# Kernel tuning notes

Hardware: AMD Instinct MI355X
Metric: run time of the kernel (lower is better)

Reference implementation:

```python
import jax, jax.numpy as jnp
import numpy as np
from jax import lax

H = 250  # hidden size of all LSTM layers


def _lstm_layer(x, Wih, Whh, bih, bhh):
    """Single-layer LSTM over time-major x [T, in], batch=1 folded away.
    PyTorch gate order: i, f, g, o. Returns hidden states [T, H]."""
    b = bih + bhh
    # Precompute input projections for all timesteps (parallel GEMM)
    xW = x @ Wih.T + b  # [T, 4H]

    def step(carry, xw_t):
        h, c = carry
        gates = xw_t + h @ Whh.T  # [4H]
        i, f, g, o = jnp.split(gates, 4)
        i = jax.nn.sigmoid(i)
        f = jax.nn.sigmoid(f)
        g = jnp.tanh(g)
        o = jax.nn.sigmoid(o)
        c = f * c + i * g
        h = o * jnp.tanh(c)
        return (h, c), h

    h0 = jnp.zeros((Whh.shape[1],), x.dtype)
    (_, _), hs = lax.scan(step, (h0, h0), xW)
    return hs  # [T, H]


def setup_inputs() -> dict:
    key = jax.random.key(0)
    ks = jax.random.split(key, 16)
    T, D = 8192, 1
    s = 1.0 / np.sqrt(H)  # PyTorch default uniform(-1/sqrt(H), 1/sqrt(H))
    u = lambda k, shape: jax.random.uniform(k, shape, jnp.float32, -s, s)
    inp = {
        "input_seq": jax.random.normal(ks[0], (T, D), jnp.float32),
        # lstm (2 layers), layer 0: input_size=1
        "Wih0": u(ks[1], (4 * H, D)), "Whh0": u(ks[2], (4 * H, H)),
        "bih0": u(ks[3], (4 * H,)), "bhh0": u(ks[4], (4 * H,)),
        # lstm layer 1: input=H
        "Wih1": u(ks[5], (4 * H, H)), "Whh1": u(ks[6], (4 * H, H)),
        "bih1": u(ks[7], (4 * H,)), "bhh1": u(ks[8], (4 * H,)),
        # lstm_1 (1 layer): input=H
        "Wih2": u(ks[9], (4 * H, H)), "Whh2": u(ks[10], (4 * H, H)),
        "bih2": u(ks[11], (4 * H,)), "bhh2": u(ks[12], (4 * H,)),
        # final linear H -> 1
        "Wl": u(ks[13], (1, H)), "bl": u(ks[14], (1,)),
    }
    return inp


def reference(input_seq, Wih0, Whh0, bih0, bhh0, Wih1, Whh1, bih1, bhh1,
              Wih2, Whh2, bih2, bhh2, Wl, bl):
    T = input_seq.shape[0]
    x = input_seq.reshape(T, -1)            # [T, 1] (batch=1 squeezed)
    h0 = _lstm_layer(x, Wih0, Whh0, bih0, bhh0)   # stacked LSTM layer 0
    h1 = _lstm_layer(h0, Wih1, Whh1, bih1, bhh1)  # layer 1 (dropout=0.2 inactive at eval)
    h2 = _lstm_layer(h1, Wih2, Whh2, bih2, bhh2)  # second LSTM module
    preds = h2 @ Wl.T + bl                  # [T, 1]
    return preds[-1]                        # [1]
```

## Files before the change

kernel.cpp:

```cpp
#include <hip/hip_runtime.h>
#include <cstdint>

#define HDIM 250
#define GDIM 1000
#define CH   64
#define PP   4
#define HRING 4
#define XRING 4
#define RPAD 1024
#define NTH  512

#define W_LDS_QPT 18
#define LDSW_BYTES (W_LDS_QPT * NTH * 16)
#define HSEG 144
#define HBUF (4 * HSEG)
#define HB_BASE LDSW_BYTES
#define RED_BASE (HB_BASE + 2 * HBUF)
#define SMEM_BYTES (RED_BASE + 1024)

typedef _Float16 f16x2 __attribute__((ext_vector_type(2)));

__device__ __forceinline__ float fdot2u(uint32_t w, uint32_t h, float acc) {
#if defined(__has_builtin) && __has_builtin(__builtin_amdgcn_fdot2)
  return __builtin_amdgcn_fdot2(__builtin_bit_cast(f16x2, w),
                                __builtin_bit_cast(f16x2, h), acc, false);
#else
  f16x2 wv = __builtin_bit_cast(f16x2, w), hv = __builtin_bit_cast(f16x2, h);
  return acc + (float)wv[0] * (float)hv[0] + (float)wv[1] * (float)hv[1];
#endif
}

__device__ __forceinline__ uint32_t pkh2(float a, float b) {
  f16x2 p; p[0] = (_Float16)a; p[1] = (_Float16)b;
  return __builtin_bit_cast(uint32_t, p);
}

__device__ __forceinline__ uint4 pack8q(const float* rp, int c0) {
  float c[8];
#pragma unroll
  for (int u = 0; u < 8; ++u) {
    int col = c0 + u;
    c[u] = (rp && col < HDIM) ? rp[col] : 0.f;
  }
  uint4 r;
  r.x = pkh2(c[0], c[1]); r.y = pkh2(c[2], c[3]);
  r.z = pkh2(c[4], c[5]); r.w = pkh2(c[6], c[7]);
  return r;
}

__device__ __forceinline__ float sigm(float x) {
  return 1.f / (1.f + exp2f(-1.44269504088896341f * x));
}
__device__ __forceinline__ float tanh_(float x) {
  float e = exp2f(2.88539008177792681f * x);
  return 1.f - 2.f / (e + 1.f);
}

template <int CTRL>
__device__ __forceinline__ float dppq(float v) {
  return __builtin_bit_cast(
      float, __builtin_amdgcn_update_dpp(0, __builtin_bit_cast(int, v), CTRL,
                                         0xF, 0xF, true));
}

__device__ __forceinline__ constexpr int kv_count(int r) { return r < 6 ? 6 : 5; }
__device__ __forceinline__ constexpr int wv_idx(int r, int k) {
  return r < 6 ? r * 6 + k : 36 + (r - 6) * 5 + k;
}
__device__ __forceinline__ constexpr int wl_idx(int r, int k) {
  return r < 6 ? r * 2 + (k - 6) : 12 + (r - 6) * 3 + (k - 5);
}

__device__ __forceinline__ void step_barrier() {
  asm volatile("s_waitcnt lgkmcnt(0)\n\ts_barrier" ::: "memory");
}

#define F_HCNT(F, li)     (F)[(li)]
#define F_XWCON(F, li)    (F)[2 + (li)]
#define F_HDONE(F, li, p) (F)[4 + (li) * PP + (p)]
#define F_XWRDY(F, li, c) (F)[16 + (li) * 128 + (c)]

__device__ __forceinline__ int aload(int* p) {
  return __hip_atomic_load(p, __ATOMIC_RELAXED, __HIP_MEMORY_SCOPE_AGENT);
}
__device__ __forceinline__ void arel(int* p, int v) {
  __hip_atomic_store(p, v, __ATOMIC_RELEASE, __HIP_MEMORY_SCOPE_AGENT);
}
__device__ __forceinline__ void acq_fence() {
  __builtin_amdgcn_fence(__ATOMIC_ACQUIRE, "agent");
}
__device__ __forceinline__ void spin_ge(int* p, int tgt) {
  unsigned n = 0;
  while (aload(p) < tgt) {
    __builtin_amdgcn_s_sleep(2);
    if (++n > 200000000u) return;
  }
}

__global__ void lstm_init(const float* __restrict__ Wih1, const float* __restrict__ bih1,
                          const float* __restrict__ bhh1, const float* __restrict__ Wih2,
                          const float* __restrict__ bih2, const float* __restrict__ bhh2,
                          float* __restrict__ WT, float* __restrict__ BV) {
  int idx = blockIdx.x * blockDim.x + threadIdx.x;
  int stride = gridDim.x * blockDim.x;
  for (int i = idx; i < 2 * HDIM * RPAD; i += stride) {
    int li = i / (HDIM * RPAD);
    int rem = i - li * HDIM * RPAD;
    int j = rem / RPAD, r = rem - j * RPAD;
    const float* W = li ? Wih2 : Wih1;
    WT[i] = (r < GDIM) ? W[r * HDIM + j] : 0.f;
  }
  for (int i = idx; i < 2 * RPAD; i += stride) {
    int li = i >> 10, r = i & 1023;
    const float* bi = li ? bih2 : bih1;
    const float* bh = li ? bhh2 : bhh1;
    BV[i] = (r < GDIM) ? bi[r] + bh[r] : 0.f;
  }
}

__global__ __launch_bounds__(512, 2) void lstm_main(
    const float* __restrict__ x, const float* __restrict__ Wih0,
    const float* __restrict__ bih0, const float* __restrict__ bhh0,
    const float* __restrict__ Whh0, const float* __restrict__ Whh1,
    const float* __restrict__ Whh2, const float* __restrict__ Wl,
    const float* __restrict__ bl, int* __restrict__ F,
    const float* __restrict__ WT, const float* __restrict__ BV,
    float* __restrict__ hRing, float* __restrict__ xwRing,
    float* __restrict__ out, int T) {
  extern __shared__ char smem[];
  const int tid = threadIdx.x;
  const int bid = blockIdx.x;
  const int NC = T / CH;

  if (bid < 3) {
    const int L = bid;
    const int grp = tid >> 2, sl = tid & 3;
    const bool lead = (sl < 2);
    const int uu = 2 * grp + sl;

    const float* Whh = (L == 0) ? Whh0 : (L == 1) ? Whh1 : Whh2;
    uint4 wv[46];
    {
#pragma unroll
      for (int r = 0; r < 8; ++r) {
        const int w = r >> 2, gate = r & 3;
        const int u = 2 * grp + w;
        const float* rp = (u < HDIM) ? (Whh + (size_t)(gate * HDIM + u) * HDIM) : nullptr;
#pragma unroll
        for (int k = 0; k < 8; ++k) {
          uint4 q = pack8q(rp, sl * 64 + k * 8);
          if (k < kv_count(r)) wv[wv_idx(r, k)] = q;
          else *(uint4*)(smem + (size_t)(wl_idx(r, k) * NTH + tid) * 16) = q;
        }
      }
    }
    for (int i = tid; i < (2 * HBUF) / 4; i += NTH)
      *(uint32_t*)(smem + HB_BASE + 4 * i) = 0u;
    __syncthreads();

    const float* xwBase = xwRing + (size_t)(L > 0 ? L - 1 : 0) * XRING * CH * RPAD;
    float* hBase = hRing + (size_t)L * HRING * CH * HDIM;
    float c_st = 0.f, h_last = 0.f;

    for (int tt = 0; tt < T; ++tt) {
      const int tc = tt & (CH - 1);
      const int c = tt >> 6;
      if (tc == 0) {
        if (tid == 0) {
          if (L > 0) spin_ge(&F_XWRDY(F, L - 1, c), 1);
          if (L < 2 && c >= HRING) {
            int cc = c - HRING;
            spin_ge(&F_HDONE(F, L, cc % PP), cc + 1);
          }
          acq_fence();
        }
        __syncthreads();
      }

      float xw0 = 0.f, xw1 = 0.f, xw2 = 0.f, xw3 = 0.f;
      if (lead && uu < HDIM) {
        if (L == 0) {
          float xt = x[tt];
          xw0 = fmaf(xt, Wih0[uu], bih0[uu] + bhh0[uu]);
          xw1 = fmaf(xt, Wih0[250 + uu], bih0[250 + uu] + bhh0[250 + uu]);
          xw2 = fmaf(xt, Wih0[500 + uu], bih0[500 + uu] + bhh0[500 + uu]);
          xw3 = fmaf(xt, Wih0[750 + uu], bih0[750 + uu] + bhh0[750 + uu]);
        } else {
          const float* xp = xwBase + (size_t)(c & (XRING - 1)) * CH * RPAD +
                            (size_t)tc * RPAD;
          xw0 = xp[uu]; xw1 = xp[250 + uu]; xw2 = xp[500 + uu]; xw3 = xp[750 + uu];
        }
      }

      step_barrier();

      const char* hb = smem + HB_BASE + (tt & 1) * HBUF + sl * HSEG;
      float acc[8] = {0.f, 0.f, 0.f, 0.f, 0.f, 0.f, 0.f, 0.f};
#pragma unroll
      for (int k = 0; k < 8; ++k) {
        const uint4 hq = *(const uint4*)(hb + k * 16);
#pragma unroll
        for (int r = 0; r < 8; ++r) {
          uint4 wq = (k < kv_count(r))
                         ? wv[wv_idx(r, k)]
                         : *(const uint4*)(smem + (size_t)(wl_idx(r, k) * NTH + tid) * 16);
          acc[r] = fdot2u(wq.x, hq.x, acc[r]);
          acc[r] = fdot2u(wq.y, hq.y, acc[r]);
          acc[r] = fdot2u(wq.z, hq.z, acc[r]);
          acc[r] = fdot2u(wq.w, hq.w, acc[r]);
        }
      }
#pragma unroll
      for (int r = 0; r < 8; ++r) {
        acc[r] += dppq<0xB1>(acc[r]);
        acc[r] += dppq<0x4E>(acc[r]);
      }

      if (lead) {
        const int of = sl * 4;
        float gi = acc[of + 0] + xw0, gf = acc[of + 1] + xw1;
        float gG = acc[of + 2] + xw2, go = acc[of + 3] + xw3;
        float ii = sigm(gi), ff = sigm(gf), tg = tanh_(gG), oo = sigm(go);
        c_st = ff * c_st + ii * tg;
        float hn = oo * tanh_(c_st);
        h_last = hn;
        float hOther = dppq<0xB1>(hn);
        if (sl == 0) {
          char* hw = smem + HB_BASE + ((tt + 1) & 1) * HBUF + (uu >> 6) * HSEG +
                     (uu & 63) * 2;
          *(uint32_t*)hw = pkh2(hn, hOther);
          if (L < 2 && uu < HDIM) {
            float2 hp; hp.x = hn; hp.y = hOther;
            *(float2*)(hBase + (size_t)(c & (HRING - 1)) * CH * HDIM +
                       (size_t)tc * HDIM + uu) = hp;
          }
        }
      }

      if (tc == CH - 1) {
        __syncthreads();
        if (tid == 0) {
          if (L < 2) arel(&F_HCNT(F, L), c + 1);
          if (L > 0) arel(&F_XWCON(F, L - 1), c + 1);
        }
      }
    }

    if (L == 2) {
      float* red = (float*)(smem + RED_BASE);
      if (lead && uu < HDIM) red[uu] = h_last;
      __syncthreads();
      if (tid == 0) {
        float s = bl[0];
        for (int j = 0; j < HDIM; ++j) s += red[j] * Wl[j];
        out[0] = s;
      }
    }
  } else {
    const int li = (bid - 3) / PP;
    const int p = (bid - 3) % PP;
    float* ldsH = (float*)smem;
    const int lane = tid & 63, wid = tid >> 6;
    const float* WTl = WT + (size_t)li * HDIM * RPAD;
    const float* BVl = BV + (size_t)li * RPAD;

    for (int c = p; c < NC; c += PP) {
      if (tid == 0) {
        spin_ge(&F_HCNT(F, li), c + 1);
        if (c >= XRING) spin_ge(&F_XWCON(F, li), c - XRING + 1);
        acq_fence();
      }
      __syncthreads();
      const float* hsrc = hRing + (size_t)li * HRING * CH * HDIM +
                          (size_t)(c & (HRING - 1)) * CH * HDIM;
      for (int t = wid; t < CH; t += 8)
        for (int j = lane; j < HDIM; j += 64)
          ldsH[t * 257 + j] = hsrc[t * HDIM + j];
      __syncthreads();
      if (tid == 0) arel(&F_HDONE(F, li, p), c + 1);

      float* xdst = xwRing + (size_t)li * XRING * CH * RPAD +
                    (size_t)(c & (XRING - 1)) * CH * RPAD;
      const int rb0 = wid * 128;
      for (int grpq = 0; grpq < 16; ++grpq) {
        const int rb = rb0 + grpq * 8;
        float acc[8];
#pragma unroll
        for (int u = 0; u < 8; ++u) acc[u] = 0.f;
        const float* wp = WTl + rb;
        float4 wa = *(const float4*)(wp);
        float4 wb = *(const float4*)(wp + 4);
        for (int j = 0; j < HDIM; ++j) {
          int jn = (j + 1 < HDIM) ? j + 1 : HDIM - 1;
          float4 na = *(const float4*)(wp + (size_t)jn * RPAD);
          float4 nb = *(const float4*)(wp + (size_t)jn * RPAD + 4);
          float hj = ldsH[lane * 257 + j];
          acc[0] = fmaf(wa.x, hj, acc[0]); acc[1] = fmaf(wa.y, hj, acc[1]);
          acc[2] = fmaf(wa.z, hj, acc[2]); acc[3] = fmaf(wa.w, hj, acc[3]);
          acc[4] = fmaf(wb.x, hj, acc[4]); acc[5] = fmaf(wb.y, hj, acc[5]);
          acc[6] = fmaf(wb.z, hj, acc[6]); acc[7] = fmaf(wb.w, hj, acc[7]);
          wa = na; wb = nb;
        }
#pragma unroll
        for (int u = 0; u < 8; ++u) {
          int r = rb + u;
          if (r < GDIM) xdst[(size_t)lane * RPAD + r] = acc[u] + BVl[r];
        }
      }
      __syncthreads();
      if (tid == 0) arel(&F_XWRDY(F, li, c), 1);
    }
  }
}

extern "C" void kernel_launch(void* const* d_in, const int* in_sizes, int n_in,
                              void* d_out, int out_size, void* d_ws, size_t ws_size,
                              hipStream_t stream) {
  const float* x    = (const float*)d_in[0];
  const float* Wih0 = (const float*)d_in[1];
  const float* Whh0 = (const float*)d_in[2];
  const float* bih0 = (const float*)d_in[3];
  const float* bhh0 = (const float*)d_in[4];
  const float* Wih1 = (const float*)d_in[5];
  const float* Whh1 = (const float*)d_in[6];
  const float* bih1 = (const float*)d_in[7];
  const float* bhh1 = (const float*)d_in[8];
  const float* Wih2 = (const float*)d_in[9];
  const float* Whh2 = (const float*)d_in[10];
  const float* bih2 = (const float*)d_in[11];
  const float* bhh2 = (const float*)d_in[12];
  const float* Wl   = (const float*)d_in[13];
  const float* bl   = (const float*)d_in[14];
  const int T = in_sizes[0];

  char* ws = (char*)d_ws;
  int*   F   = (int*)ws;
  float* WT  = (float*)(ws + 4096);
  float* BV  = (float*)(ws + 4096 + 2048000);
  float* hR  = (float*)(ws + 4096 + 2048000 + 8192);
  float* xwR = (float*)(ws + 4096 + 2048000 + 8192 + 512000);

  hipMemsetAsync(F, 0, 4096, stream);
  lstm_init<<<256, 256, 0, stream>>>(Wih1, bih1, bhh1, Wih2, bih2, bhh2, WT, BV);
  hipFuncSetAttribute(reinterpret_cast<const void*>(lstm_main),
                      hipFuncAttributeMaxDynamicSharedMemorySize, SMEM_BYTES);
  lstm_main<<<3 + 2 * PP, 512, SMEM_BYTES, stream>>>(
      x, Wih0, bih0, bhh0, Whh0, Whh1, Whh2, Wl, bl, F, WT, BV, hR, xwR,
      (float*)d_out, T);
}
```

Measured before the change: 21.01 ms.

## Double threads per block so each recurrent thread owns one gate row

After: 19.85 ms. -5.5%, faster.

```diff
diff --git a/kernel.cpp b/kernel.cpp
--- a/kernel.cpp
+++ b/kernel.cpp
@@ -8,10 +8,10 @@
 #define HRING 4
 #define XRING 4
 #define RPAD 1024
-#define NTH  512
-
-#define W_LDS_QPT 18
-#define LDSW_BYTES (W_LDS_QPT * NTH * 16)
+#define NTH  1024
+
+#define LQ_N 8
+#define LDSW_BYTES (LQ_N * NTH * 16)
 #define HSEG 144
 #define HBUF (4 * HSEG)
 #define HB_BASE LDSW_BYTES
@@ -48,12 +48,19 @@
   return r;
 }
 
+__device__ __forceinline__ float rcpf_(float x) {
+#if defined(__has_builtin) && __has_builtin(__builtin_amdgcn_rcpf)
+  return __builtin_amdgcn_rcpf(x);
+#else
+  return 1.f / x;
+#endif
+}
 __device__ __forceinline__ float sigm(float x) {
-  return 1.f / (1.f + exp2f(-1.44269504088896341f * x));
+  return rcpf_(1.f + exp2f(-1.44269504088896341f * x));
 }
 __device__ __forceinline__ float tanh_(float x) {
   float e = exp2f(2.88539008177792681f * x);
-  return 1.f - 2.f / (e + 1.f);
+  return 1.f - 2.f * rcpf_(e + 1.f);
 }
 
 template <int CTRL>
@@ -61,14 +68,6 @@
   return __builtin_bit_cast(
       float, __builtin_amdgcn_update_dpp(0, __builtin_bit_cast(int, v), CTRL,
                                          0xF, 0xF, true));
-}
-
-__device__ __forceinline__ constexpr int kv_count(int r) { return r < 6 ? 6 : 5; }
-__device__ __forceinline__ constexpr int wv_idx(int r, int k) {
-  return r < 6 ? r * 6 + k : 36 + (r - 6) * 5 + k;
-}
-__device__ __forceinline__ constexpr int wl_idx(int r, int k) {
-  return r < 6 ? r * 2 + (k - 6) : 12 + (r - 6) * 3 + (k - 5);
 }
 
 __device__ __forceinline__ void step_barrier() {
@@ -118,7 +117,7 @@
   }
 }
 
-__global__ __launch_bounds__(512, 2) void lstm_main(
+__global__ void __launch_bounds__(NTH) lstm_main(
     const float* __restrict__ x, const float* __restrict__ Wih0,
     const float* __restrict__ bih0, const float* __restrict__ bhh0,
     const float* __restrict__ Whh0, const float* __restrict__ Whh1,
@@ -134,26 +133,36 @@
 
   if (bid < 3) {
     const int L = bid;
-    const int grp = tid >> 2, sl = tid & 3;
-    const bool lead = (sl < 2);
-    const int uu = 2 * grp + sl;
+    const int u = tid >> 2, sl = tid & 3;
+    const bool uok = (u < HDIM);
+    const int r_abs = sl * HDIM + u;
 
     const float* Whh = (L == 0) ? Whh0 : (L == 1) ? Whh1 : Whh2;
-    uint4 wv[46];
-    {
-#pragma unroll
-      for (int r = 0; r < 8; ++r) {
-        const int w = r >> 2, gate = r & 3;
-        const int u = 2 * grp + w;
-        const float* rp = (u < HDIM) ? (Whh + (size_t)(gate * HDIM + u) * HDIM) : nullptr;
-#pragma unroll
-        for (int k = 0; k < 8; ++k) {
-          uint4 q = pack8q(rp, sl * 64 + k * 8);
-          if (k < kv_count(r)) wv[wv_idx(r, k)] = q;
-          else *(uint4*)(smem + (size_t)(wl_idx(r, k) * NTH + tid) * 16) = q;
-        }
-      }
+    char* lw = smem + tid * 16;
+#define LWADDR(lq) (lw + (size_t)(lq) * (NTH * 16))
+#define ROWP(r) (uok ? (Whh + ((size_t)(r) * HDIM + u) * HDIM) : (const float*)nullptr)
+
+    uint4 w00, w01, w02, w03, w04, w05;
+    uint4 w10, w11, w12, w13, w14, w15;
+    uint4 w20, w21, w22, w23, w24, w25;
+    uint4 w30, w31, w32, w33, w34, w35;
+#define INITROW(r)                                          \
+  w##r##0 = pack8q(ROWP(r), sl * 64 + 0);                   \
+  w##r##1 = pack8q(ROWP(r), sl * 64 + 8);                   \
+  w##r##2 = pack8q(ROWP(r), sl * 64 + 16);                  \
+  w##r##3 = pack8q(ROWP(r), sl * 64 + 24);                  \
+  w##r##4 = pack8q(ROWP(r), sl * 64 + 32);                  \
+  w##r##5 = pack8q(ROWP(r), sl * 64 + 40);                  \
+  *(uint4*)LWADDR(2 * (r)) = pack8q(ROWP(r), sl * 64 + 48); \
+  *(uint4*)LWADDR(2 * (r) + 1) = pack8q(ROWP(r), sl * 64 + 56);
+    INITROW(0) INITROW(1) INITROW(2) INITROW(3)
+
+    float w0_ = 0.f, b0_ = 0.f;
+    if (L == 0 && uok) {
+      w0_ = Wih0[r_abs];
+      b0_ = bih0[r_abs] + bhh0[r_abs];
     }
+
     for (int i = tid; i < (2 * HBUF) / 4; i += NTH)
       *(uint32_t*)(smem + HB_BASE + 4 * i) = 0u;
     __syncthreads();
@@ -177,64 +186,70 @@
         __syncthreads();
       }
 
-      float xw0 = 0.f, xw1 = 0.f, xw2 = 0.f, xw3 = 0.f;
-      if (lead && uu < HDIM) {
+      float xw = 0.f;
+      if (uok) {
         if (L == 0) {
-          float xt = x[tt];
-          xw0 = fmaf(xt, Wih0[uu], bih0[uu] + bhh0[uu]);
-          xw1 = fmaf(xt, Wih0[250 + uu], bih0[250 + uu] + bhh0[250 + uu]);
-          xw2 = fmaf(xt, Wih0[500 + uu], bih0[500 + uu] + bhh0[500 + uu]);
-          xw3 = fmaf(xt, Wih0[750 + uu], bih0[750 + uu] + bhh0[750 + uu]);
+          xw = fmaf(x[tt], w0_, b0_);
         } else {
           const float* xp = xwBase + (size_t)(c & (XRING - 1)) * CH * RPAD +
                             (size_t)tc * RPAD;
-          xw0 = xp[uu]; xw1 = xp[250 + uu]; xw2 = xp[500 + uu]; xw3 = xp[750 + uu];
-        }
-      }
-
-      step_barrier();
+          xw = xp[r_abs];
+        }
+      }
 
       const char* hb = smem + HB_BASE + (tt & 1) * HBUF + sl * HSEG;
-      float acc[8] = {0.f, 0.f, 0.f, 0.f, 0.f, 0.f, 0.f, 0.f};
-#pragma unroll
-      for (int k = 0; k < 8; ++k) {
-        const uint4 hq = *(const uint4*)(hb + k * 16);
-#pragma unroll
-        for (int r = 0; r < 8; ++r) {
-          uint4 wq = (k < kv_count(r))
-                         ? wv[wv_idx(r, k)]
-                         : *(const uint4*)(smem + (size_t)(wl_idx(r, k) * NTH + tid) * 16);
-          acc[r] = fdot2u(wq.x, hq.x, acc[r]);
-          acc[r] = fdot2u(wq.y, hq.y, acc[r]);
-          acc[r] = fdot2u(wq.z, hq.z, acc[r]);
-          acc[r] = fdot2u(wq.w, hq.w, acc[r]);
-        }
-      }
-#pragma unroll
-      for (int r = 0; r < 8; ++r) {
-        acc[r] += dppq<0xB1>(acc[r]);
-        acc[r] += dppq<0x4E>(acc[r]);
-      }
-
-      if (lead) {
-        const int of = sl * 4;
-        float gi = acc[of + 0] + xw0, gf = acc[of + 1] + xw1;
-        float gG = acc[of + 2] + xw2, go = acc[of + 3] + xw3;
-        float ii = sigm(gi), ff = sigm(gf), tg = tanh_(gG), oo = sigm(go);
-        c_st = ff * c_st + ii * tg;
-        float hn = oo * tanh_(c_st);
-        h_last = hn;
-        float hOther = dppq<0xB1>(hn);
-        if (sl == 0) {
-          char* hw = smem + HB_BASE + ((tt + 1) & 1) * HBUF + (uu >> 6) * HSEG +
-                     (uu & 63) * 2;
-          *(uint32_t*)hw = pkh2(hn, hOther);
-          if (L < 2 && uu < HDIM) {
-            float2 hp; hp.x = hn; hp.y = hOther;
-            *(float2*)(hBase + (size_t)(c & (HRING - 1)) * CH * HDIM +
-                       (size_t)tc * HDIM + uu) = hp;
-          }
-        }
+      float a0 = 0.f, a1 = 0.f, a2 = 0.f, a3 = 0.f;
+#define FD4(W_, H_, A_)                \
+  A_ = fdot2u((W_).x, (H_).x, A_);     \
+  A_ = fdot2u((W_).y, (H_).y, A_);     \
+  A_ = fdot2u((W_).z, (H_).z, A_);     \
+  A_ = fdot2u((W_).w, (H_).w, A_);
+#define DOTK(k)                                      \
+  {                                                  \
+    const uint4 hq = *(const uint4*)(hb + (k) * 16); \
+    FD4(w0##k, hq, a0)                               \
+    FD4(w1##k, hq, a1)                               \
+    FD4(w2##k, hq, a2)                               \
+    FD4(w3##k, hq, a3)                               \
+  }
+      DOTK(0) DOTK(1) DOTK(2) DOTK(3) DOTK(4) DOTK(5)
+      {
+        const uint4 hq = *(const uint4*)(hb + 96);
+        uint4 q;
+        q = *(const uint4*)LWADDR(0); FD4(q, hq, a0)
+        q = *(const uint4*)LWADDR(2); FD4(q, hq, a1)
+        q = *(const uint4*)LWADDR(4); FD4(q, hq, a2)
+        q = *(const uint4*)LWADDR(6); FD4(q, hq, a3)
+      }
+      {
+        const uint4 hq = *(const uint4*)(hb + 112);
+        uint4 q;
+        q = *(const uint4*)LWADDR(1); FD4(q, hq, a0)
+        q = *(const uint4*)LWADDR(3); FD4(q, hq, a1)
+        q = *(const uint4*)LWADDR(5); FD4(q, hq, a2)
+        q = *(const uint4*)LWADDR(7); FD4(q, hq, a3)
+      }
+
+      a0 += (sl == 0) ? xw : 0.f;
+      a1 += (sl == 1) ? xw : 0.f;
+      a2 += (sl == 2) ? xw : 0.f;
+      a3 += (sl == 3) ? xw : 0.f;
+      a0 += dppq<0xB1>(a0); a0 += dppq<0x4E>(a0);
+      a1 += dppq<0xB1>(a1); a1 += dppq<0x4E>(a1);
+      a2 += dppq<0xB1>(a2); a2 += dppq<0x4E>(a2);
+      a3 += dppq<0xB1>(a3); a3 += dppq<0x4E>(a3);
+
+      float ii = sigm(a0), ff = sigm(a1), tg = tanh_(a2), oo = sigm(a3);
+      c_st = ff * c_st + ii * tg;
+      float hn = oo * tanh_(c_st);
+      h_last = hn;
+
+      if (sl == 0 && uok) {
+        char* hw = smem + HB_BASE + ((tt + 1) & 1) * HBUF + (u >> 6) * HSEG +
+                   (u & 63) * 2;
+        *(_Float16*)hw = (_Float16)hn;
+        if (L < 2)
+          hBase[(size_t)(c & (HRING - 1)) * CH * HDIM + (size_t)tc * HDIM + u] = hn;
       }
 
       if (tc == CH - 1) {
@@ -243,12 +258,14 @@
           if (L < 2) arel(&F_HCNT(F, L), c + 1);
           if (L > 0) arel(&F_XWCON(F, L - 1), c + 1);
         }
+      } else {
+        step_barrier();
       }
     }
 
     if (L == 2) {
       float* red = (float*)(smem + RED_BASE);
-      if (lead && uu < HDIM) red[uu] = h_last;
+      if (sl == 0 && uok) red[u] = h_last;
       __syncthreads();
       if (tid == 0) {
         float s = bl[0];
@@ -273,7 +290,7 @@
       __syncthreads();
       const float* hsrc = hRing + (size_t)li * HRING * CH * HDIM +
                           (size_t)(c & (HRING - 1)) * CH * HDIM;
-      for (int t = wid; t < CH; t += 8)
+      for (int t = wid; t < CH; t += 16)
         for (int j = lane; j < HDIM; j += 64)
           ldsH[t * 257 + j] = hsrc[t * HDIM + j];
       __syncthreads();
@@ -281,30 +298,30 @@
 
       float* xdst = xwRing + (size_t)li * XRING * CH * RPAD +
                     (size_t)(c & (XRING - 1)) * CH * RPAD;
-      const int rb0 = wid * 128;
-      for (int grpq = 0; grpq < 16; ++grpq) {
+      const int rb0 = wid * 64;
+      for (int grpq = 0; grpq < 8; ++grpq) {
         const int rb = rb0 + grpq * 8;
         float acc[8];
 #pragma unroll
-        for (int u = 0; u < 8; ++u) acc[u] = 0.f;
+        for (int uq = 0; uq < 8; ++uq) acc[uq] = 0.f;
         const float* wp = WTl + rb;
-        float4 wa = *(const float4*)(wp);
-        float4 wb = *(const float4*)(wp + 4);
+        float4 wa4 = *(const float4*)(wp);
+        float4 wb4 = *(const float4*)(wp + 4);
         for (int j = 0; j < HDIM; ++j) {
           int jn = (j + 1 < HDIM) ? j + 1 : HDIM - 1;
           float4 na = *(const float4*)(wp + (size_t)jn * RPAD);
           float4 nb = *(const float4*)(wp + (size_t)jn * RPAD + 4);
           float hj = ldsH[lane * 257 + j];
-          acc[0] = fmaf(wa.x, hj, acc[0]); acc[1] = fmaf(wa.y, hj, acc[1]);
-          acc[2] = fmaf(wa.z, hj, acc[2]); acc[3] = fmaf(wa.w, hj, acc[3]);
-          acc[4] = fmaf(wb.x, hj, acc[4]); acc[5] = fmaf(wb.y, hj, acc[5]);
-          acc[6] = fmaf(wb.z, hj, acc[6]); acc[7] = fmaf(wb.w, hj, acc[7]);
-          wa = na; wb = nb;
+          acc[0] = fmaf(wa4.x, hj, acc[0]); acc[1] = fmaf(wa4.y, hj, acc[1]);
+          acc[2] = fmaf(wa4.z, hj, acc[2]); acc[3] = fmaf(wa4.w, hj, acc[3]);
+          acc[4] = fmaf(wb4.x, hj, acc[4]); acc[5] = fmaf(wb4.y, hj, acc[5]);
+          acc[6] = fmaf(wb4.z, hj, acc[6]); acc[7] = fmaf(wb4.w, hj, acc[7]);
+          wa4 = na; wb4 = nb;
         }
 #pragma unroll
-        for (int u = 0; u < 8; ++u) {
-          int r = rb + u;
-          if (r < GDIM) xdst[(size_t)lane * RPAD + r] = acc[u] + BVl[r];
+        for (int uq = 0; uq < 8; ++uq) {
+          int r = rb + uq;
+          if (r < GDIM) xdst[(size_t)lane * RPAD + r] = acc[uq] + BVl[r];
         }
       }
       __syncthreads();
@@ -344,7 +361,7 @@
   lstm_init<<<256, 256, 0, stream>>>(Wih1, bih1, bhh1, Wih2, bih2, bhh2, WT, BV);
   hipFuncSetAttribute(reinterpret_cast<const void*>(lstm_main),
                       hipFuncAttributeMaxDynamicSharedMemorySize, SMEM_BYTES);
-  lstm_main<<<3 + 2 * PP, 512, SMEM_BYTES, stream>>>(
+  lstm_main<<<3 + 2 * PP, NTH, SMEM_BYTES, stream>>>(
       x, Wih0, bih0, bhh0, Whh0, Whh1, Whh2, Wl, bl, F, WT, BV, hR, xwR,
       (float*)d_out, T);
 }
```
